# Kernel optimization log

Hardware: AMD Instinct MI355X
Metric: run time of the kernel (lower is better)

The kernel has to match this reference:

```python
import jax, jax.numpy as jnp
import numpy as np

BITS = 4
MAXQ = (1 << BITS) - 1          # 15
PACK = 32 // BITS               # 8 values per int32
GROUP = 128
CLIPMIN = 1e-5
CLIPMAX = 1e4


def _unpack_rows(qweight, infeatures):
    # qweight: [in/PACK, out] int32; values packed along the row (infeatures) dim.
    shifts = (jnp.arange(PACK, dtype=jnp.int32) * BITS)[None, :, None]   # [1,PACK,1]
    w = (qweight[:, None, :] >> shifts) & MAXQ                            # [in/PACK, PACK, out]
    return w.reshape(-1, qweight.shape[1])[:infeatures].astype(jnp.float32)


def setup_inputs() -> dict:
    key = jax.random.key(0)
    k1, k2, k3, k4, k5 = jax.random.split(key, 5)
    infeatures, outfeatures, tokens = 4096, 4096, 2048
    num_groups = infeatures // GROUP
    x = jax.random.normal(k1, (tokens, infeatures), dtype=jnp.float32)
    # positive scales, well inside [CLIPMIN, CLIPMAX]
    scales = jax.random.uniform(k2, (num_groups, outfeatures), dtype=jnp.float32,
                                minval=0.005, maxval=0.02)
    # zero points roughly centered in the quant range [0, 15]
    zero_points = jax.random.uniform(k3, (num_groups, outfeatures), dtype=jnp.float32,
                                     minval=0.0, maxval=float(MAXQ))
    bias = jax.random.normal(k4, (outfeatures,), dtype=jnp.float32)
    qweight = jax.random.randint(k5, (infeatures // PACK, outfeatures),
                                 jnp.iinfo(jnp.int32).min, jnp.iinfo(jnp.int32).max,
                                 dtype=jnp.int32)
    return {"x": x, "scales": scales, "zero_points": zero_points,
            "bias": bias, "qweight": qweight}


def reference(x, scales, zero_points, bias, qweight):
    infeatures = x.shape[-1]
    out_f = scales.shape[1]
    num_groups = scales.shape[0]
    w = _unpack_rows(qweight, infeatures)                       # [in, out] fp32 in [0,15]
    s = jnp.clip(scales, CLIPMIN, CLIPMAX)                      # [G, out]
    z = jnp.clip(jnp.round(zero_points), 0.0, float(MAXQ))      # [G, out]
    wg = w.reshape(num_groups, GROUP, out_f)                    # [G, group, out]
    deq = ((wg - z[:, None, :]) * s[:, None, :]).reshape(infeatures, out_f)
    return x @ deq + bias
```

## Files before the change

kernel.cpp:

```cpp
#include <hip/hip_runtime.h>
#include <cstdint>
#include <cstddef>

typedef __attribute__((ext_vector_type(8))) short short8;
typedef __attribute__((ext_vector_type(4))) float floatx4;

typedef __attribute__((address_space(1))) const void gvoid_t;
typedef __attribute__((address_space(3))) void lvoid_t;

__device__ inline short f2bf(float f) {
    unsigned u = __float_as_uint(f);
    u = (u + 0x7FFFu + ((u >> 16) & 1u)) >> 16;
    return (short)u;
}

__global__ __launch_bounds__(256) void prologue_kernel(
    const float* __restrict__ x, short* __restrict__ xb, long long nx, int ncvt,
    const int* __restrict__ qw, const float* __restrict__ scales,
    const float* __restrict__ zps, short* __restrict__ deqT,
    int N, int K, int nbx)
{
    __shared__ int lds_q[32 * 65];
    const int t = threadIdx.x;

    if ((int)blockIdx.x < ncvt) {
        long long i = ((long long)blockIdx.x * 256 + t) * 8;
        if (i + 8 > nx) return;
        const float4* p = (const float4*)(x + i);
        float4 v0 = p[0];
        float4 v1 = p[1];
        short8 h;
        h[0] = f2bf(v0.x); h[1] = f2bf(v0.y); h[2] = f2bf(v0.z); h[3] = f2bf(v0.w);
        h[4] = f2bf(v1.x); h[5] = f2bf(v1.y); h[6] = f2bf(v1.z); h[7] = f2bf(v1.w);
        *(short8*)(xb + i) = h;
        return;
    }

    const int b2 = (int)blockIdx.x - ncvt;
    const int n0 = (b2 % nbx) * 64;
    const int r0 = (b2 / nbx) * 32;

    #pragma unroll
    for (int v = 0; v < 2; ++v) {
        int idx = t + v * 256;
        int row = idx >> 4;
        int c4  = (idx & 15) * 4;
        const int4 q4 = *(const int4*)(qw + (size_t)(r0 + row) * N + n0 + c4);
        int base = row * 65 + c4;
        lds_q[base + 0] = q4.x;
        lds_q[base + 1] = q4.y;
        lds_q[base + 2] = q4.z;
        lds_q[base + 3] = q4.w;
    }
    __syncthreads();

    const int L  = t & 63;
    const int w  = t >> 6;
    const int rq = L & 31;
    const int hi = L >> 5;
    const int g  = (r0 + rq) >> 4;

    #pragma unroll
    for (int it = 0; it < 8; ++it) {
        const int p  = w * 8 + it;
        const int nl = 2 * p + hi;

        float s = scales[(size_t)g * N + n0 + nl];
        s = fminf(fmaxf(s, 1e-5f), 1e4f);
        float z = rintf(zps[(size_t)g * N + n0 + nl]);
        z = fminf(fmaxf(z, 0.0f), 15.0f);

        const int q = lds_q[rq * 65 + nl];
        short8 h;
        #pragma unroll
        for (int j = 0; j < 8; ++j) {
            float f = (float)((q >> (4 * j)) & 15);
            h[j] = f2bf((f - z) * s);
        }
        *(short8*)(deqT + (size_t)(n0 + nl) * K + (size_t)(r0 + rq) * 8) = h;
    }
}

#define BM 128
#define BN 128
#define BK 64

__global__ __launch_bounds__(256) void gemm_bf16_bt(
    const short* __restrict__ A, const short* __restrict__ Bt,
    const float* __restrict__ bias, float* __restrict__ C,
    int M, int N, int K)
{
    __shared__ __align__(16) short a_lds[2][BM * BK];
    __shared__ __align__(16) short b_lds[2][BN * BK];

    const int t  = threadIdx.x;
    const int L  = t & 63;
    const int w  = t >> 6;

    const int nbn = N / BN;
    const int id  = blockIdx.y * gridDim.x + blockIdx.x;
    const int xcd = id & 7;
    const int loc = id >> 3;
    const int gsz = nbn / 8;
    const int nt  = xcd * gsz + (loc % gsz);
    const int mt  = loc / gsz;
    const int m0  = mt * BM;
    const int n0  = nt * BN;

    const int wm = (w & 1) * 64;
    const int wn = (w >> 1) * 64;

    floatx4 acc[4][4] = {};

    const int sr = L >> 3;
    const int sc = L & 7;
    const int gc = sc ^ sr;
    const short* ag = A  + (size_t)(m0 + w * 8 + sr) * K + gc * 8;
    const short* bg = Bt + (size_t)(n0 + w * 8 + sr) * K + gc * 8;
    const int dst = (w * 8) * BK;

    const int NK = K / BK;

    #pragma unroll
    for (int i = 0; i < 4; ++i) {
        __builtin_amdgcn_global_load_lds(
            (gvoid_t*)(ag + (size_t)i * 32 * K),
            (lvoid_t*)(&a_lds[0][dst + i * 32 * BK]), 16, 0, 0);
        __builtin_amdgcn_global_load_lds(
            (gvoid_t*)(bg + (size_t)i * 32 * K),
            (lvoid_t*)(&b_lds[0][dst + i * 32 * BK]), 16, 0, 0);
    }

    for (int ti = 0; ti < NK; ++ti) {
        const int cur = ti & 1;
        __syncthreads();

        if (ti + 1 < NK) {
            const int kn = (ti + 1) * BK;
            #pragma unroll
            for (int i = 0; i < 4; ++i) {
                __builtin_amdgcn_global_load_lds(
                    (gvoid_t*)(ag + (size_t)i * 32 * K + kn),
                    (lvoid_t*)(&a_lds[cur ^ 1][dst + i * 32 * BK]), 16, 0, 0);
                __builtin_amdgcn_global_load_lds(
                    (gvoid_t*)(bg + (size_t)i * 32 * K + kn),
                    (lvoid_t*)(&b_lds[cur ^ 1][dst + i * 32 * BK]), 16, 0, 0);
            }
        }

        #pragma unroll
        for (int s = 0; s < 2; ++s) {
            const int p = (s * 4 + (L >> 4)) ^ (L & 7);
            short8 af[4], bfr[4];
            #pragma unroll
            for (int i = 0; i < 4; ++i)
                af[i] = *(const short8*)(&a_lds[cur][(wm + 16 * i + (L & 15)) * BK + p * 8]);
            #pragma unroll
            for (int j = 0; j < 4; ++j)
                bfr[j] = *(const short8*)(&b_lds[cur][(wn + 16 * j + (L & 15)) * BK + p * 8]);
            #pragma unroll
            for (int i = 0; i < 4; ++i) {
                #pragma unroll
                for (int j = 0; j < 4; ++j)
                    acc[i][j] = __builtin_amdgcn_mfma_f32_16x16x32_bf16(
                        af[i], bfr[j], acc[i][j], 0, 0, 0);
            }
        }
    }

    float bv[4];
    #pragma unroll
    for (int j = 0; j < 4; ++j)
        bv[j] = bias[n0 + wn + 16 * j + (L & 15)];
    const int col0 = n0 + wn + (L & 15);
    #pragma unroll
    for (int i = 0; i < 4; ++i) {
        const int row0 = m0 + wm + 16 * i + (L >> 4) * 4;
        #pragma unroll
        for (int r = 0; r < 4; ++r) {
            float* outr = C + (size_t)(row0 + r) * N + col0;
            #pragma unroll
            for (int j = 0; j < 4; ++j)
                outr[16 * j] = acc[i][j][r] + bv[j];
        }
    }
}

extern "C" void kernel_launch(void* const* d_in, const int* in_sizes, int n_in,
                              void* d_out, int out_size, void* d_ws, size_t ws_size,
                              hipStream_t stream)
{
    const float* x      = (const float*)d_in[0];
    const float* scales = (const float*)d_in[1];
    const float* zps    = (const float*)d_in[2];
    const float* bias   = (const float*)d_in[3];
    const int*   qw     = (const int*)d_in[4];

    const int N = in_sizes[3];
    const int G = in_sizes[1] / N;
    const int K = G * 128;
    const int M = in_sizes[0] / K;

    short* xb   = (short*)d_ws;
    short* deqT = xb + (size_t)M * K;
    float* out  = (float*)d_out;

    const long long nx = (long long)M * K;
    const int ncvt = (int)(nx / 2048);
    const int nbx  = N / 64;
    const int ndq  = nbx * (K / 256);

    prologue_kernel<<<ncvt + ndq, 256, 0, stream>>>(
        x, xb, nx, ncvt, qw, scales, zps, deqT, N, K, nbx);
    gemm_bf16_bt<<<dim3(N / BN, M / BM), 256, 0, stream>>>(xb, deqT, bias, out, M, N, K);
}
```

Before: 166.4 us.

## Restructure GEMM into 8-wave 128x256 tile with interleaved barrier/priority schedule

Widens the GEMM block tile to 128x256 and uses 512 threads (8 waves) per block over a flattened 1D grid with XCD-aware tile mapping. The main loop becomes a prefetch-two-ahead double buffer: LDS fragment reads are split into four phases, each fenced with lgkmcnt waits, block barriers and s_setprio around the MFMA bursts, and the next tile's loads are issued mid-iteration. The goal is to hide global and LDS latency behind MFMA work and raise data reuse per block. In exchange it needs more LDS per block (likely one block per CU), many more barriers, and only 256 blocks in total, which reduces tail flexibility.

```diff
diff --git a/kernel.cpp b/kernel.cpp
--- a/kernel.cpp
+++ b/kernel.cpp
@@ -82,10 +82,15 @@
 }
 
 #define BM 128
-#define BN 128
+#define BN 256
 #define BK 64
 
-__global__ __launch_bounds__(256) void gemm_bf16_bt(
+#define LGKM0_FENCE() do { \
+    asm volatile("s_waitcnt lgkmcnt(0)" ::: "memory"); \
+    __builtin_amdgcn_sched_barrier(0); \
+} while (0)
+
+__global__ __launch_bounds__(512, 2) void gemm_bf16_bt(
     const short* __restrict__ A, const short* __restrict__ Bt,
     const float* __restrict__ bias, float* __restrict__ C,
     int M, int N, int K)
@@ -93,19 +98,25 @@
     __shared__ __align__(16) short a_lds[2][BM * BK];
     __shared__ __align__(16) short b_lds[2][BN * BK];
 
-    const int t  = threadIdx.x;
-    const int L  = t & 63;
-    const int w  = t >> 6;
+    const int t = threadIdx.x;
+    const int L = t & 63;
+    const int w = t >> 6;
 
     const int nbn = N / BN;
-    const int id  = blockIdx.y * gridDim.x + blockIdx.x;
-    const int xcd = id & 7;
-    const int loc = id >> 3;
-    const int gsz = nbn / 8;
-    const int nt  = xcd * gsz + (loc % gsz);
-    const int mt  = loc / gsz;
-    const int m0  = mt * BM;
-    const int n0  = nt * BN;
+    const int id  = blockIdx.x;
+    int nt, mt;
+    if ((nbn & 7) == 0) {
+        const int xcd = id & 7;
+        const int loc = id >> 3;
+        const int gsz = nbn >> 3;
+        nt = xcd * gsz + (loc % gsz);
+        mt = loc / gsz;
+    } else {
+        nt = id % nbn;
+        mt = id / nbn;
+    }
+    const int m0 = mt * BM;
+    const int n0 = nt * BN;
 
     const int wm = (w & 1) * 64;
     const int wn = (w >> 1) * 64;
@@ -117,65 +128,118 @@
     const int gc = sc ^ sr;
     const short* ag = A  + (size_t)(m0 + w * 8 + sr) * K + gc * 8;
     const short* bg = Bt + (size_t)(n0 + w * 8 + sr) * K + gc * 8;
-    const int dst = (w * 8) * BK;
-
-    const int NK = K / BK;
-
+    const int adst = (w * 8) * BK;
+
+    const int NT = K / BK;
+
+    const int l15 = L & 15, l4 = L >> 4, l7 = L & 7;
+    const int p0 = l4 ^ l7;
+    const int p1 = (4 + l4) ^ l7;
+
+#define STAGE(kt_, buf_) do { \
+    const size_t ko_ = (size_t)(kt_) * BK; \
+    __builtin_amdgcn_global_load_lds((gvoid_t*)(ag + ko_), \
+        (lvoid_t*)(&a_lds[buf_][adst]), 16, 0, 0); \
+    __builtin_amdgcn_global_load_lds((gvoid_t*)(ag + (size_t)64 * K + ko_), \
+        (lvoid_t*)(&a_lds[buf_][adst + 64 * BK]), 16, 0, 0); \
+    __builtin_amdgcn_global_load_lds((gvoid_t*)(bg + ko_), \
+        (lvoid_t*)(&b_lds[buf_][adst]), 16, 0, 0); \
+    __builtin_amdgcn_global_load_lds((gvoid_t*)(bg + (size_t)64 * K + ko_), \
+        (lvoid_t*)(&b_lds[buf_][adst + 64 * BK]), 16, 0, 0); \
+    __builtin_amdgcn_global_load_lds((gvoid_t*)(bg + (size_t)128 * K + ko_), \
+        (lvoid_t*)(&b_lds[buf_][adst + 128 * BK]), 16, 0, 0); \
+    __builtin_amdgcn_global_load_lds((gvoid_t*)(bg + (size_t)192 * K + ko_), \
+        (lvoid_t*)(&b_lds[buf_][adst + 192 * BK]), 16, 0, 0); \
+} while (0)
+
+    STAGE(0, 0);
+    STAGE(1, 1);
+    asm volatile("s_waitcnt vmcnt(6)" ::: "memory");
+    __builtin_amdgcn_s_barrier();
+
+    for (int ti = 0; ti < NT; ++ti) {
+        const int cur = ti & 1;
+        short8 a0[4], a1[4], b0f[4], b1f[4];
+
+        #pragma unroll
+        for (int i = 0; i < 4; ++i)
+            a0[i] = *(const short8*)(&a_lds[cur][(wm + 16 * i + l15) * BK + p0 * 8]);
+        #pragma unroll
+        for (int j = 0; j < 2; ++j)
+            b0f[j] = *(const short8*)(&b_lds[cur][(wn + 16 * j + l15) * BK + p0 * 8]);
+        LGKM0_FENCE();
+        __builtin_amdgcn_s_barrier();
+        __builtin_amdgcn_s_setprio(1);
+        #pragma unroll
+        for (int i = 0; i < 4; ++i) {
+            acc[i][0] = __builtin_amdgcn_mfma_f32_16x16x32_bf16(a0[i], b0f[0], acc[i][0], 0, 0, 0);
+            acc[i][1] = __builtin_amdgcn_mfma_f32_16x16x32_bf16(a0[i], b0f[1], acc[i][1], 0, 0, 0);
+        }
+        __builtin_amdgcn_s_setprio(0);
+        __builtin_amdgcn_s_barrier();
+
+        #pragma unroll
+        for (int j = 2; j < 4; ++j)
+            b0f[j] = *(const short8*)(&b_lds[cur][(wn + 16 * j + l15) * BK + p0 * 8]);
+        LGKM0_FENCE();
+        __builtin_amdgcn_s_barrier();
+        __builtin_amdgcn_s_setprio(1);
+        #pragma unroll
+        for (int i = 0; i < 4; ++i) {
+            acc[i][2] = __builtin_amdgcn_mfma_f32_16x16x32_bf16(a0[i], b0f[2], acc[i][2], 0, 0, 0);
+            acc[i][3] = __builtin_amdgcn_mfma_f32_16x16x32_bf16(a0[i], b0f[3], acc[i][3], 0, 0, 0);
+        }
+        __builtin_amdgcn_s_setprio(0);
+        __builtin_amdgcn_s_barrier();
+
+        #pragma unroll
+        for (int i = 0; i < 4; ++i)
+            a1[i] = *(const short8*)(&a_lds[cur][(wm + 16 * i + l15) * BK + p1 * 8]);
+        #pragma unroll
+        for (int j = 0; j < 2; ++j)
+            b1f[j] = *(const short8*)(&b_lds[cur][(wn + 16 * j + l15) * BK + p1 * 8]);
+        LGKM0_FENCE();
+        __builtin_amdgcn_s_barrier();
+        __builtin_amdgcn_s_setprio(1);
+        #pragma unroll
+        for (int i = 0; i < 4; ++i) {
+            acc[i][0] = __builtin_amdgcn_mfma_f32_16x16x32_bf16(a1[i], b1f[0], acc[i][0], 0, 0, 0);
+            acc[i][1] = __builtin_amdgcn_mfma_f32_16x16x32_bf16(a1[i], b1f[1], acc[i][1], 0, 0, 0);
+        }
+        __builtin_amdgcn_s_setprio(0);
+        __builtin_amdgcn_s_barrier();
+
+        #pragma unroll
+        for (int j = 2; j < 4; ++j)
+            b1f[j] = *(const short8*)(&b_lds[cur][(wn + 16 * j + l15) * BK + p1 * 8]);
+        LGKM0_FENCE();
+        __builtin_amdgcn_s_barrier();
+        if (ti + 2 < NT) {
+            STAGE(ti + 2, cur);
+        }
+        __builtin_amdgcn_s_setprio(1);
+        #pragma unroll
+        for (int i = 0; i < 4; ++i) {
+            acc[i][2] = __builtin_amdgcn_mfma_f32_16x16x32_bf16(a1[i], b1f[2], acc[i][2], 0, 0, 0);
+            acc[i][3] = __builtin_amdgcn_mfma_f32_16x16x32_bf16(a1[i], b1f[3], acc[i][3], 0, 0, 0);
+        }
+        __builtin_amdgcn_s_setprio(0);
+        if (ti + 2 < NT) {
+            asm volatile("s_waitcnt vmcnt(6)" ::: "memory");
+        } else if (ti + 1 < NT) {
+            asm volatile("s_waitcnt vmcnt(0)" ::: "memory");
+        }
+        __builtin_amdgcn_s_barrier();
+    }
+
+    float bv[4];
+    #pragma unroll
+    for (int j = 0; j < 4; ++j)
+        bv[j] = bias[n0 + wn + 16 * j + l15];
+    const int col0 = n0 + wn + l15;
     #pragma unroll
     for (int i = 0; i < 4; ++i) {
-        __builtin_amdgcn_global_load_lds(
-            (gvoid_t*)(ag + (size_t)i * 32 * K),
-            (lvoid_t*)(&a_lds[0][dst + i * 32 * BK]), 16, 0, 0);
-        __builtin_amdgcn_global_load_lds(
-            (gvoid_t*)(bg + (size_t)i * 32 * K),
-            (lvoid_t*)(&b_lds[0][dst + i * 32 * BK]), 16, 0, 0);
-    }
-
-    for (int ti = 0; ti < NK; ++ti) {
-        const int cur = ti & 1;
-        __syncthreads();
-
-        if (ti + 1 < NK) {
-            const int kn = (ti + 1) * BK;
-            #pragma unroll
-            for (int i = 0; i < 4; ++i) {
-                __builtin_amdgcn_global_load_lds(
-                    (gvoid_t*)(ag + (size_t)i * 32 * K + kn),
-                    (lvoid_t*)(&a_lds[cur ^ 1][dst + i * 32 * BK]), 16, 0, 0);
-                __builtin_amdgcn_global_load_lds(
-                    (gvoid_t*)(bg + (size_t)i * 32 * K + kn),
-                    (lvoid_t*)(&b_lds[cur ^ 1][dst + i * 32 * BK]), 16, 0, 0);
-            }
-        }
-
-        #pragma unroll
-        for (int s = 0; s < 2; ++s) {
-            const int p = (s * 4 + (L >> 4)) ^ (L & 7);
-            short8 af[4], bfr[4];
-            #pragma unroll
-            for (int i = 0; i < 4; ++i)
-                af[i] = *(const short8*)(&a_lds[cur][(wm + 16 * i + (L & 15)) * BK + p * 8]);
-            #pragma unroll
-            for (int j = 0; j < 4; ++j)
-                bfr[j] = *(const short8*)(&b_lds[cur][(wn + 16 * j + (L & 15)) * BK + p * 8]);
-            #pragma unroll
-            for (int i = 0; i < 4; ++i) {
-                #pragma unroll
-                for (int j = 0; j < 4; ++j)
-                    acc[i][j] = __builtin_amdgcn_mfma_f32_16x16x32_bf16(
-                        af[i], bfr[j], acc[i][j], 0, 0, 0);
-            }
-        }
-    }
-
-    float bv[4];
-    #pragma unroll
-    for (int j = 0; j < 4; ++j)
-        bv[j] = bias[n0 + wn + 16 * j + (L & 15)];
-    const int col0 = n0 + wn + (L & 15);
-    #pragma unroll
-    for (int i = 0; i < 4; ++i) {
-        const int row0 = m0 + wm + 16 * i + (L >> 4) * 4;
+        const int row0 = m0 + wm + 16 * i + l4 * 4;
         #pragma unroll
         for (int r = 0; r < 4; ++r) {
             float* outr = C + (size_t)(row0 + r) * N + col0;
@@ -212,5 +276,6 @@
 
     prologue_kernel<<<ncvt + ndq, 256, 0, stream>>>(
         x, xb, nx, ncvt, qw, scales, zps, deqT, N, K, nbx);
-    gemm_bf16_bt<<<dim3(N / BN, M / BM), 256, 0, stream>>>(xb, deqT, bias, out, M, N, K);
-}
+    gemm_bf16_bt<<<dim3((M / BM) * (N / BN)), 512, 0, stream>>>(
+        xb, deqT, bias, out, M, N, K);
+}
```

New measurement: 198.7 us. 19.4% more time.

## Replace GEMM with 256x256 split-K kernel using atomic accumulation

Applied to the files above, without the earlier changes.

Replaces the 128x128 double-buffered GEMM with a 512-thread 256x256-tile kernel that splits K in two and accumulates into the output with atomicAdd. The prologue now also pre-fills the output with the bias. The new kernel uses a 4-stage LDS ring, interleaved staging, manual waitcnt/sched barriers and setprio around MFMA bursts. This is meant to raise arithmetic intensity and keep the MFMA units fed. In exchange it adds fp32 atomic traffic on the output, an extra bias-write pass, and non-deterministic summation order.

```diff
diff --git a/kernel.cpp b/kernel.cpp
--- a/kernel.cpp
+++ b/kernel.cpp
@@ -18,13 +18,15 @@
     const float* __restrict__ x, short* __restrict__ xb, long long nx, int ncvt,
     const int* __restrict__ qw, const float* __restrict__ scales,
     const float* __restrict__ zps, short* __restrict__ deqT,
-    int N, int K, int nbx)
+    int N, int K, int nbx, int ndq,
+    const float* __restrict__ bias, float* __restrict__ C, long long mn)
 {
     __shared__ int lds_q[32 * 65];
     const int t = threadIdx.x;
-
-    if ((int)blockIdx.x < ncvt) {
-        long long i = ((long long)blockIdx.x * 256 + t) * 8;
+    const int bid = (int)blockIdx.x;
+
+    if (bid < ncvt) {
+        long long i = ((long long)bid * 256 + t) * 8;
         if (i + 8 > nx) return;
         const float4* p = (const float4*)(x + i);
         float4 v0 = p[0];
@@ -36,154 +38,206 @@
         return;
     }
 
-    const int b2 = (int)blockIdx.x - ncvt;
-    const int n0 = (b2 % nbx) * 64;
-    const int r0 = (b2 / nbx) * 32;
-
+    if (bid < ncvt + ndq) {
+        const int b2 = bid - ncvt;
+        const int n0 = (b2 % nbx) * 64;
+        const int r0 = (b2 / nbx) * 32;
+
+        #pragma unroll
+        for (int v = 0; v < 2; ++v) {
+            int idx = t + v * 256;
+            int row = idx >> 4;
+            int c4  = (idx & 15) * 4;
+            const int4 q4 = *(const int4*)(qw + (size_t)(r0 + row) * N + n0 + c4);
+            int base = row * 65 + c4;
+            lds_q[base + 0] = q4.x;
+            lds_q[base + 1] = q4.y;
+            lds_q[base + 2] = q4.z;
+            lds_q[base + 3] = q4.w;
+        }
+        __syncthreads();
+
+        const int L  = t & 63;
+        const int w  = t >> 6;
+        const int rq = L & 31;
+        const int hi = L >> 5;
+        const int g  = (r0 + rq) >> 4;
+
+        #pragma unroll
+        for (int it = 0; it < 8; ++it) {
+            const int p  = w * 8 + it;
+            const int nl = 2 * p + hi;
+
+            float s = scales[(size_t)g * N + n0 + nl];
+            s = fminf(fmaxf(s, 1e-5f), 1e4f);
+            float z = rintf(zps[(size_t)g * N + n0 + nl]);
+            z = fminf(fmaxf(z, 0.0f), 15.0f);
+
+            const int q = lds_q[rq * 65 + nl];
+            short8 h;
+            #pragma unroll
+            for (int j = 0; j < 8; ++j) {
+                float f = (float)((q >> (4 * j)) & 15);
+                h[j] = f2bf((f - z) * s);
+            }
+            *(short8*)(deqT + (size_t)(n0 + nl) * K + (size_t)(r0 + rq) * 8) = h;
+        }
+        return;
+    }
+
+    long long i = ((long long)(bid - ncvt - ndq) * 256 + t) * 8;
+    if (i + 8 > mn) return;
+    const int col = (int)(i % (long long)N);
+    const float4 b0 = *(const float4*)(bias + col);
+    const float4 b1 = *(const float4*)(bias + col + 4);
+    float4* o = (float4*)(C + i);
+    o[0] = b0; o[1] = b1;
+}
+
+__global__ __launch_bounds__(512, 2) void gemm_bf16_sk(
+    const short* __restrict__ A, const short* __restrict__ Bt,
+    float* __restrict__ C, int M, int N, int K)
+{
+    __shared__ __align__(16) short a_lds[4][128 * 64];
+    __shared__ __align__(16) short b_lds[4][128 * 64];
+
+    const int t = threadIdx.x;
+    const int L = t & 63;
+    const int w = t >> 6;
+
+    const int mtiles = M >> 8, ntiles = N >> 8;
+    int mt, nt, sk;
+    if (mtiles == 8 && ntiles == 16) {
+        const int id = blockIdx.x;
+        const int loc = id >> 3;
+        mt = loc & 7;
+        nt = (id & 7) * 2 + ((loc >> 3) & 1);
+        sk = (loc >> 4) & 1;
+    } else {
+        const int tpg = mtiles * ntiles;
+        sk = blockIdx.x / tpg;
+        const int r = blockIdx.x % tpg;
+        nt = r % ntiles; mt = r / ntiles;
+    }
+    const int KH = K >> 1;
+    const int m0 = mt << 8, n0 = nt << 8, kb = sk * KH;
+    const int NT = KH / 64;
+
+    const int hA  = w & 1;
+    const int wn  = (w >> 1) * 64;
+    const int rBb = wn & 127;
+    const int hB  = w >> 2;
+    const int l15 = L & 15, l4 = L >> 4, l7 = L & 7;
+    const int p0 = l4 ^ l7, p1 = (4 + l4) ^ l7;
+    const int sr = L >> 3, sc = L & 7, gc = sc ^ sr;
+
+    const short* agp = A  + (size_t)(m0 + w * 8 + sr) * K + kb + gc * 8;
+    const short* bgp = Bt + (size_t)(n0 + w * 8 + sr) * K + kb + gc * 8;
+    const int dstw = (w * 8) * 64;
+
+    floatx4 acc[8][4] = {};
+
+#define STG_A(tn_, h_) do { \
+    const int st_ = (2 * (tn_) + (h_)) & 3; \
+    const size_t ko_ = (size_t)(tn_) * 64; \
+    __builtin_amdgcn_global_load_lds((gvoid_t*)(agp + (size_t)((h_) * 128) * K + ko_), \
+        (lvoid_t*)(&a_lds[st_][dstw]), 16, 0, 0); \
+    __builtin_amdgcn_global_load_lds((gvoid_t*)(agp + (size_t)((h_) * 128 + 64) * K + ko_), \
+        (lvoid_t*)(&a_lds[st_][dstw + 64 * 64]), 16, 0, 0); \
+} while (0)
+
+#define STG_B(tn_, h_) do { \
+    const int st_ = (2 * (tn_) + (h_)) & 3; \
+    const size_t ko_ = (size_t)(tn_) * 64; \
+    __builtin_amdgcn_global_load_lds((gvoid_t*)(bgp + (size_t)((h_) * 128) * K + ko_), \
+        (lvoid_t*)(&b_lds[st_][dstw]), 16, 0, 0); \
+    __builtin_amdgcn_global_load_lds((gvoid_t*)(bgp + (size_t)((h_) * 128 + 64) * K + ko_), \
+        (lvoid_t*)(&b_lds[st_][dstw + 64 * 64]), 16, 0, 0); \
+} while (0)
+
+#define MFMA16(j_, bx0_, bx1_) do { \
+    __builtin_amdgcn_s_setprio(1); \
+    _Pragma("unroll") \
+    for (int i_ = 0; i_ < 8; ++i_) { \
+        acc[i_][j_] = __builtin_amdgcn_mfma_f32_16x16x32_bf16(ah0[i_], bx0_, acc[i_][j_], 0, 0, 0); \
+        acc[i_][j_] = __builtin_amdgcn_mfma_f32_16x16x32_bf16(ah1[i_], bx1_, acc[i_][j_], 0, 0, 0); \
+    } \
+    __builtin_amdgcn_s_setprio(0); \
+} while (0)
+
+    STG_A(0, 0); STG_A(0, 1); STG_B(0, 0); STG_B(0, 1);
+
+    for (int ti = 0; ti < NT; ++ti) {
+        const bool g = (ti + 1 < NT);
+        const short* Ab = &a_lds[(2 * ti + hA) & 3][0];
+        const short* Bb = &b_lds[(2 * ti + hB) & 3][0];
+        short8 ah0[8], ah1[8];
+        short8 b00, b01, b10, b11, b20, b21, b30, b31;
+
+        if (g) {
+            STG_A(ti + 1, 0);
+            asm volatile("s_waitcnt vmcnt(2)" ::: "memory");
+        } else {
+            asm volatile("s_waitcnt vmcnt(0)" ::: "memory");
+        }
+        __builtin_amdgcn_s_barrier();
+        #pragma unroll
+        for (int i = 0; i < 8; ++i) {
+            ah0[i] = *(const short8*)(Ab + (16 * i + l15) * 64 + p0 * 8);
+            ah1[i] = *(const short8*)(Ab + (16 * i + l15) * 64 + p1 * 8);
+        }
+        b00 = *(const short8*)(Bb + (rBb + l15) * 64 + p0 * 8);
+        b01 = *(const short8*)(Bb + (rBb + l15) * 64 + p1 * 8);
+        __builtin_amdgcn_sched_barrier(0);
+        b10 = *(const short8*)(Bb + (rBb + 16 + l15) * 64 + p0 * 8);
+        b11 = *(const short8*)(Bb + (rBb + 16 + l15) * 64 + p1 * 8);
+        asm volatile("s_waitcnt lgkmcnt(2)" ::: "memory");
+        __builtin_amdgcn_sched_barrier(0);
+        MFMA16(0, b00, b01);
+        __builtin_amdgcn_s_barrier();
+
+        b20 = *(const short8*)(Bb + (rBb + 32 + l15) * 64 + p0 * 8);
+        b21 = *(const short8*)(Bb + (rBb + 32 + l15) * 64 + p1 * 8);
+        if (g) STG_A(ti + 1, 1);
+        __builtin_amdgcn_s_barrier();
+        asm volatile("s_waitcnt lgkmcnt(2)" ::: "memory");
+        __builtin_amdgcn_sched_barrier(0);
+        MFMA16(1, b10, b11);
+        __builtin_amdgcn_s_barrier();
+
+        b30 = *(const short8*)(Bb + (rBb + 48 + l15) * 64 + p0 * 8);
+        b31 = *(const short8*)(Bb + (rBb + 48 + l15) * 64 + p1 * 8);
+        if (g) STG_B(ti + 1, 0);
+        __builtin_amdgcn_s_barrier();
+        asm volatile("s_waitcnt lgkmcnt(2)" ::: "memory");
+        __builtin_amdgcn_sched_barrier(0);
+        MFMA16(2, b20, b21);
+        __builtin_amdgcn_s_barrier();
+
+        if (g) STG_B(ti + 1, 1);
+        __builtin_amdgcn_s_barrier();
+        asm volatile("s_waitcnt lgkmcnt(0)" ::: "memory");
+        __builtin_amdgcn_sched_barrier(0);
+        MFMA16(3, b30, b31);
+        if (g) asm volatile("s_waitcnt vmcnt(4)" ::: "memory");
+        __builtin_amdgcn_s_barrier();
+    }
+
+    const int col0 = n0 + wn + l15;
     #pragma unroll
-    for (int v = 0; v < 2; ++v) {
-        int idx = t + v * 256;
-        int row = idx >> 4;
-        int c4  = (idx & 15) * 4;
-        const int4 q4 = *(const int4*)(qw + (size_t)(r0 + row) * N + n0 + c4);
-        int base = row * 65 + c4;
-        lds_q[base + 0] = q4.x;
-        lds_q[base + 1] = q4.y;
-        lds_q[base + 2] = q4.z;
-        lds_q[base + 3] = q4.w;
-    }
-    __syncthreads();
-
-    const int L  = t & 63;
-    const int w  = t >> 6;
-    const int rq = L & 31;
-    const int hi = L >> 5;
-    const int g  = (r0 + rq) >> 4;
-
-    #pragma unroll
-    for (int it = 0; it < 8; ++it) {
-        const int p  = w * 8 + it;
-        const int nl = 2 * p + hi;
-
-        float s = scales[(size_t)g * N + n0 + nl];
-        s = fminf(fmaxf(s, 1e-5f), 1e4f);
-        float z = rintf(zps[(size_t)g * N + n0 + nl]);
-        z = fminf(fmaxf(z, 0.0f), 15.0f);
-
-        const int q = lds_q[rq * 65 + nl];
-        short8 h;
-        #pragma unroll
-        for (int j = 0; j < 8; ++j) {
-            float f = (float)((q >> (4 * j)) & 15);
-            h[j] = f2bf((f - z) * s);
-        }
-        *(short8*)(deqT + (size_t)(n0 + nl) * K + (size_t)(r0 + rq) * 8) = h;
-    }
-}
-
-#define BM 128
-#define BN 128
-#define BK 64
-
-__global__ __launch_bounds__(256) void gemm_bf16_bt(
-    const short* __restrict__ A, const short* __restrict__ Bt,
-    const float* __restrict__ bias, float* __restrict__ C,
-    int M, int N, int K)
-{
-    __shared__ __align__(16) short a_lds[2][BM * BK];
-    __shared__ __align__(16) short b_lds[2][BN * BK];
-
-    const int t  = threadIdx.x;
-    const int L  = t & 63;
-    const int w  = t >> 6;
-
-    const int nbn = N / BN;
-    const int id  = blockIdx.y * gridDim.x + blockIdx.x;
-    const int xcd = id & 7;
-    const int loc = id >> 3;
-    const int gsz = nbn / 8;
-    const int nt  = xcd * gsz + (loc % gsz);
-    const int mt  = loc / gsz;
-    const int m0  = mt * BM;
-    const int n0  = nt * BN;
-
-    const int wm = (w & 1) * 64;
-    const int wn = (w >> 1) * 64;
-
-    floatx4 acc[4][4] = {};
-
-    const int sr = L >> 3;
-    const int sc = L & 7;
-    const int gc = sc ^ sr;
-    const short* ag = A  + (size_t)(m0 + w * 8 + sr) * K + gc * 8;
-    const short* bg = Bt + (size_t)(n0 + w * 8 + sr) * K + gc * 8;
-    const int dst = (w * 8) * BK;
-
-    const int NK = K / BK;
-
-    #pragma unroll
-    for (int i = 0; i < 4; ++i) {
-        __builtin_amdgcn_global_load_lds(
-            (gvoid_t*)(ag + (size_t)i * 32 * K),
-            (lvoid_t*)(&a_lds[0][dst + i * 32 * BK]), 16, 0, 0);
-        __builtin_amdgcn_global_load_lds(
-            (gvoid_t*)(bg + (size_t)i * 32 * K),
-            (lvoid_t*)(&b_lds[0][dst + i * 32 * BK]), 16, 0, 0);
-    }
-
-    for (int ti = 0; ti < NK; ++ti) {
-        const int cur = ti & 1;
-        __syncthreads();
-
-        if (ti + 1 < NK) {
-            const int kn = (ti + 1) * BK;
-            #pragma unroll
-            for (int i = 0; i < 4; ++i) {
-                __builtin_amdgcn_global_load_lds(
-                    (gvoid_t*)(ag + (size_t)i * 32 * K + kn),
-                    (lvoid_t*)(&a_lds[cur ^ 1][dst + i * 32 * BK]), 16, 0, 0);
-                __builtin_amdgcn_global_load_lds(
-                    (gvoid_t*)(bg + (size_t)i * 32 * K + kn),
-                    (lvoid_t*)(&b_lds[cur ^ 1][dst + i * 32 * BK]), 16, 0, 0);
-            }
-        }
-
-        #pragma unroll
-        for (int s = 0; s < 2; ++s) {
-            const int p = (s * 4 + (L >> 4)) ^ (L & 7);
-            short8 af[4], bfr[4];
-            #pragma unroll
-            for (int i = 0; i < 4; ++i)
-                af[i] = *(const short8*)(&a_lds[cur][(wm + 16 * i + (L & 15)) * BK + p * 8]);
+    for (int i = 0; i < 8; ++i) {
+        const int row0 = m0 + hA * 128 + 16 * i + l4 * 4;
+        #pragma unroll
+        for (int r = 0; r < 4; ++r) {
+            float* cr = C + (size_t)(row0 + r) * N + col0;
             #pragma unroll
             for (int j = 0; j < 4; ++j)
-                bfr[j] = *(const short8*)(&b_lds[cur][(wn + 16 * j + (L & 15)) * BK + p * 8]);
-            #pragma unroll
-            for (int i = 0; i < 4; ++i) {
-                #pragma unroll
-                for (int j = 0; j < 4; ++j)
-                    acc[i][j] = __builtin_amdgcn_mfma_f32_16x16x32_bf16(
-                        af[i], bfr[j], acc[i][j], 0, 0, 0);
-            }
-        }
-    }
-
-    float bv[4];
-    #pragma unroll
-    for (int j = 0; j < 4; ++j)
-        bv[j] = bias[n0 + wn + 16 * j + (L & 15)];
-    const int col0 = n0 + wn + (L & 15);
-    #pragma unroll
-    for (int i = 0; i < 4; ++i) {
-        const int row0 = m0 + wm + 16 * i + (L >> 4) * 4;
-        #pragma unroll
-        for (int r = 0; r < 4; ++r) {
-            float* outr = C + (size_t)(row0 + r) * N + col0;
-            #pragma unroll
-            for (int j = 0; j < 4; ++j)
-                outr[16 * j] = acc[i][j][r] + bv[j];
-        }
-    }
+                atomicAdd(cr + 16 * j, acc[i][j][r]);
+        }
+    }
+#undef STG_A
+#undef STG_B
+#undef MFMA16
 }
 
 extern "C" void kernel_launch(void* const* d_in, const int* in_sizes, int n_in,
@@ -206,11 +260,14 @@
     float* out  = (float*)d_out;
 
     const long long nx = (long long)M * K;
-    const int ncvt = (int)(nx / 2048);
-    const int nbx  = N / 64;
-    const int ndq  = nbx * (K / 256);
-
-    prologue_kernel<<<ncvt + ndq, 256, 0, stream>>>(
-        x, xb, nx, ncvt, qw, scales, zps, deqT, N, K, nbx);
-    gemm_bf16_bt<<<dim3(N / BN, M / BM), 256, 0, stream>>>(xb, deqT, bias, out, M, N, K);
-}
+    const long long mn = (long long)M * N;
+    const int ncvt  = (int)(nx / 2048);
+    const int nbx   = N / 64;
+    const int ndq   = nbx * (K / 256);
+    const int nbias = (int)(mn / 2048);
+
+    prologue_kernel<<<ncvt + ndq + nbias, 256, 0, stream>>>(
+        x, xb, nx, ncvt, qw, scales, zps, deqT, N, K, nbx, ndq, bias, out, mn);
+    gemm_bf16_sk<<<2 * (M / 256) * (N / 256), 512, 0, stream>>>(
+        xb, deqT, out, M, N, K);
+}
```

After: 216.0 us. 29.8% more time.
